# Optimization experiments

Measured on AMD Instinct MI355X. Metric: run time of the kernel, lower is better.

Reference implementation:

```python
import jax, jax.numpy as jnp
import numpy as np

BZ, IN_DIM, STATE_DIM, OUT_DIM, L = 16, 512, 512, 512, 2048
INIT_SCALE = 0.5


def setup_inputs() -> dict:
    key = jax.random.key(0)
    k_u, k_a, k_b, k_c = jax.random.split(key, 4)
    u = jax.random.normal(k_u, (BZ, IN_DIM, L), dtype=jnp.float32)
    A_unconstrained = jax.random.normal(k_a, (STATE_DIM,), dtype=jnp.float32) * 0.1
    B = jax.random.normal(k_b, (STATE_DIM, IN_DIM), dtype=jnp.float32) * INIT_SCALE / np.sqrt(IN_DIM)
    C = jax.random.normal(k_c, (OUT_DIM, STATE_DIM), dtype=jnp.float32) * INIT_SCALE / np.sqrt(STATE_DIM)
    D = jnp.zeros((OUT_DIM, IN_DIM), dtype=jnp.float32)
    h0 = jnp.zeros((STATE_DIM,), dtype=jnp.float32)
    return {"u": u, "A_unconstrained": A_unconstrained, "B": B, "C": C, "D": D, "h0": h0}


def reference(u, A_unconstrained, B, C, D, h0):
    # u: (Bz, input_dim, L)
    Bz = u.shape[0]
    A_diag = -jax.nn.softplus(A_unconstrained)  # (S,)
    # Time-invariant input projection, batched over all timesteps: (L, Bz, S)
    Bu = jnp.einsum('bil,si->lbs', u, B)

    state0 = jnp.broadcast_to(h0[None, :], (Bz, h0.shape[0]))

    def step(state, bu_t):
        x_t = state * A_diag[None, :] + bu_t  # (Bz, S)
        return x_t, x_t

    _, xs = jax.lax.scan(step, state0, Bu)  # xs: (L, Bz, S)

    # Output projection: y_t = C x_t + D u_t  -> (Bz, out, L)
    Y = jnp.einsum('lbs,os->bol', xs, C) + jnp.einsum('bil,oi->bol', u, D)
    return Y
```

## Files before the change

### kernel.cpp

```cpp
#include <hip/hip_runtime.h>
#include <math.h>

typedef __bf16 bf16;
typedef __bf16 bf16x2 __attribute__((ext_vector_type(2)));
typedef __bf16 bf16x4 __attribute__((ext_vector_type(4)));
typedef __bf16 bf16x8 __attribute__((ext_vector_type(8)));
typedef float  f32x4  __attribute__((ext_vector_type(4)));

#define BZd 16
#define INd 512
#define Sd  512
#define Od  512
#define Ld  2048
#define CLd 128
#define NCd (Ld / CLd)

__device__ __forceinline__ int keyf(int r) { return (r & 3) ^ ((r >> 2) & 3); }

__global__ __launch_bounds__(256) void prep_all(const float* __restrict__ B,
                                                const float* __restrict__ C,
                                                const float* __restrict__ D,
                                                const float* __restrict__ Au,
                                                bf16* __restrict__ Bb, bf16* __restrict__ Cb,
                                                bf16* __restrict__ Db, float* __restrict__ A_diag,
                                                int* __restrict__ dfa) {
    __shared__ int sred[4];
    int bid = blockIdx.x;
    if (bid == 768) {
        #pragma unroll
        for (int r = 0; r < 2; ++r) {
            int ss = threadIdx.x + r * 256;
            float x = Au[ss];
            float sp = fmaxf(x, 0.0f) + log1pf(expf(-fabsf(x)));
            A_diag[ss] = -sp;
        }
        return;
    }
    int which = bid >> 8, lb = bid & 255;
    const float* src = which == 0 ? B : (which == 1 ? C : D);
    bf16* dst = which == 0 ? Bb : (which == 1 ? Cb : Db);
    int i = lb * 256 + threadIdx.x;
    f32x4 v = *(const f32x4*)&src[(size_t)i * 4];
    bf16x4 o = { (bf16)v[0], (bf16)v[1], (bf16)v[2], (bf16)v[3] };
    *(bf16x4*)&dst[(size_t)i * 4] = o;
    if (which == 2) {
        int nz = (v[0] != 0.f) | (v[1] != 0.f) | (v[2] != 0.f) | (v[3] != 0.f);
        unsigned long long bl = __ballot(nz);
        int wv = threadIdx.x >> 6;
        if ((threadIdx.x & 63) == 0) sred[wv] = (bl != 0ull);
        __syncthreads();
        if (threadIdx.x == 0) dfa[lb] = sred[0] | sred[1] | sred[2] | sred[3];
    }
}

__global__ __launch_bounds__(256, 2) void gemm_bu128(
    const float* __restrict__ Uf,
    const bf16* __restrict__ Bbf,
    const float* __restrict__ A_diag,
    float* __restrict__ ce,
    bf16* __restrict__ xs)
{
    constexpr int ASLOT = 128 * 32;
    constexpr int BSLOT = 128 * 32;
    __shared__ bf16 lds[2 * ASLOT + 3 * BSLOT];

    const int tid = threadIdx.x, lane = tid & 63, w = tid >> 6;

    int nwg = gridDim.x, bid = blockIdx.x;
    int cpx = nwg >> 3;
    int swz = (bid & 7) * cpx + (bid >> 3);
    int b  = swz >> 6;
    int r0 = swz & 63;
    int by = r0 >> 2;
    int bx = r0 & 3;

    const int wm = w >> 1, wn = w & 1;
    const int fr = lane & 15, g = lane >> 4;
    const int iq = tid & 7, lq = tid >> 3;

    const float* Ub = Uf + (size_t)b * INd * Ld;
    const bf16*  Bp = Bbf + (size_t)(bx * 128) * 512;

    f32x4 acc[4][4];
    #pragma unroll
    for (int i = 0; i < 4; ++i)
        #pragma unroll
        for (int j = 0; j < 4; ++j)
            acc[i][j] = (f32x4){0.f, 0.f, 0.f, 0.f};

    f32x4 areg[4];

    #define GLD16B(srcP, dstElem) __builtin_amdgcn_global_load_lds( \
        (const __attribute__((address_space(1))) void*)(srcP), \
        (__attribute__((address_space(3))) void*)&lds[dstElem], 16, 0, 0)

    auto issueA = [&](int U) {
        #pragma unroll
        for (int d = 0; d < 4; ++d)
            areg[d] = *(const f32x4*)&Ub[(size_t)(U * 32 + iq * 4 + d) * Ld + by * 128 + lq * 4];
    };
    auto writeA = [&](int U) {
        bf16* As = &lds[(U & 1) * ASLOT];
        #pragma unroll
        for (int dl = 0; dl < 4; ++dl) {
            int r = lq * 4 + dl;
            bf16x4 wv = { (bf16)areg[0][dl], (bf16)areg[1][dl], (bf16)areg[2][dl], (bf16)areg[3][dl] };
            *(bf16x4*)&As[r * 32 + (((iq >> 1) ^ keyf(r)) * 8) + (iq & 1) * 4] = wv;
        }
    };
    auto gldB = [&](int U) {
        #pragma unroll
        for (int rb = 0; rb < 2; ++rb) {
            int row = rb * 64 + (tid >> 2);
            int cs = (tid & 3) ^ keyf(row);
            GLD16B(Bp + (size_t)row * 512 + U * 32 + cs * 8,
                   2 * ASLOT + (U % 3) * BSLOT + (rb * 64 + w * 16) * 32);
        }
    };

    issueA(0);
    __builtin_amdgcn_sched_barrier(0);
    gldB(0); gldB(1);
    __builtin_amdgcn_sched_barrier(0);

    for (int U = 0; U < 16; ++U) {
        if (U < 15) { asm volatile("s_waitcnt vmcnt(2)" ::: "memory"); }
        else        { asm volatile("s_waitcnt vmcnt(0)" ::: "memory"); }
        __builtin_amdgcn_sched_barrier(0);
        writeA(U);
        asm volatile("s_waitcnt lgkmcnt(0)" ::: "memory");
        __builtin_amdgcn_sched_barrier(0);
        __builtin_amdgcn_s_barrier();
        __builtin_amdgcn_sched_barrier(0);
        if (U + 1 < 16) {
            issueA(U + 1);
            __builtin_amdgcn_sched_barrier(0);
        }
        bf16x8 av[4], bv[4];
        {
            const bf16* As = &lds[(U & 1) * ASLOT];
            const bf16* Bs = &lds[2 * ASLOT + (U % 3) * BSLOT];
            #pragma unroll
            for (int i = 0; i < 4; ++i) {
                int R = wm * 64 + i * 16 + fr;
                av[i] = *(const bf16x8*)&As[R * 32 + (g ^ keyf(R)) * 8];
            }
            #pragma unroll
            for (int j = 0; j < 4; ++j) {
                int R = wn * 64 + j * 16 + fr;
                bv[j] = *(const bf16x8*)&Bs[R * 32 + (g ^ keyf(R)) * 8];
            }
        }
        if (U + 2 < 16) {
            gldB(U + 2);
            __builtin_amdgcn_sched_barrier(0);
        }
        __builtin_amdgcn_s_setprio(1);
        #pragma unroll
        for (int i = 0; i < 4; ++i)
            #pragma unroll
            for (int j = 0; j < 4; ++j)
                acc[i][j] = __builtin_amdgcn_mfma_f32_16x16x32_bf16(av[i], bv[j], acc[i][j], 0, 0, 0);
        __builtin_amdgcn_s_setprio(0);
    }

    int n0 = bx * 128 + wn * 64 + fr;
    int m0 = by * 128 + wm * 64 + g * 4;

    __syncthreads();
    float* scf = (float*)lds;
    float Sv[4], a64j[4];
    #pragma unroll
    for (int j = 0; j < 4; ++j) {
        float a = A_diag[n0 + j * 16];
        float a2 = a * a, a4 = a2 * a2, a8 = a4 * a4, a16 = a8 * a8;
        float a32 = a16 * a16;
        a64j[j] = a32 * a32;
        float S = 0.f;
        #pragma unroll
        for (int i = 0; i < 4; ++i) {
            f32x4 v = acc[i][j];
            float e = fmaf(fmaf(fmaf(v[0], a, v[1]), a, v[2]), a, v[3]);
            float e0 = __shfl(e, fr), e1 = __shfl(e, fr + 16);
            float e2 = __shfl(e, fr + 32), e3 = __shfl(e, fr + 48);
            float E = fmaf(fmaf(fmaf(e0, a4, e1), a4, e2), a4, e3);
            S = fmaf(S, a16, E);
        }
        Sv[j] = S;
    }
    if (wm == 0 && g == 0) {
        #pragma unroll
        for (int j = 0; j < 4; ++j) scf[wn * 64 + j * 16 + fr] = Sv[j];
    }
    __syncthreads();
    if (wm == 1 && g == 0) {
        #pragma unroll
        for (int j = 0; j < 4; ++j) {
            float S0 = scf[wn * 64 + j * 16 + fr];
            ce[((size_t)b * NCd + by) * Sd + n0 + j * 16] = fmaf(S0, a64j[j], Sv[j]);
        }
    }

    bf16* out = xs + (size_t)b * Ld * Sd;
    #pragma unroll
    for (int i = 0; i < 4; ++i)
        #pragma unroll
        for (int j = 0; j < 4; ++j)
            #pragma unroll
            for (int q = 0; q < 4; ++q)
                out[(size_t)(m0 + i * 16 + q) * Sd + n0 + j * 16] = (bf16)acc[i][j][q];
    #undef GLD16B
}

template<int AREG, int SCAN>
__global__ __launch_bounds__(512, 2) void gemm8p(
    const bf16* __restrict__ Abf, size_t aBS,
    const float* __restrict__ Uf, size_t uBS,
    const bf16* __restrict__ Bbf, size_t bBS,
    const bf16* __restrict__ Dbf,
    const int* __restrict__ dfa,
    const float* __restrict__ A_diag, float* __restrict__ cePtr,
    void* __restrict__ OutV, size_t oBS, int ldOut,
    int NX, int NY)
{
    constexpr int RS   = 32;
    constexpr int ASZ  = 256 * RS;
    constexpr int SLOT = ASZ + 256 * 32;
    __shared__ bf16 lds[4 * SLOT];

    const int tid = threadIdx.x;
    const int lane = tid & 63, w = tid >> 6;

    int nwg = gridDim.x, bid = blockIdx.x;
    int cpx = nwg >> 3;
    int swz = (bid & 7) * cpx + (bid >> 3);
    int pb = NX * NY;
    int b  = swz / pb;
    int r0 = swz - b * pb;
    int by = r0 / NX;
    int bx = r0 - by * NX;

    const int wm = w >> 2, wn = w & 3;
    const int fr = lane & 15, g = lane >> 4;
    const int iq = tid & 7, lq = tid >> 3;

    const bf16*  Ab = Abf + (size_t)b * aBS + (size_t)(by * 256) * 512;
    const float* Ub = Uf ? (Uf + (size_t)b * uBS) : nullptr;
    const bf16*  Bp = Bbf + (size_t)b * bBS + (size_t)(bx * 256) * 512;

    int extra = 0;
    if (dfa) {
        int4 f = ((const int4*)dfa)[lane];
        extra = __any((f.x | f.y | f.z | f.w) != 0) ? 1 : 0;
    }

    f32x4 acc[8][4];
    #pragma unroll
    for (int i = 0; i < 8; ++i)
        #pragma unroll
        for (int j = 0; j < 4; ++j)
            acc[i][j] = (f32x4){0.f, 0.f, 0.f, 0.f};

    #define GLD16(srcP, dstElem) __builtin_amdgcn_global_load_lds( \
        (const __attribute__((address_space(1))) void*)(srcP), \
        (__attribute__((address_space(3))) void*)&lds[dstElem], 16, 0, 0)

    auto gldA = [&](int U) {
        #pragma unroll
        for (int rb = 0; rb < 2; ++rb) {
            int row = rb * 128 + (tid >> 2);
            int cs = (tid & 3) ^ keyf(row);
            GLD16(Ab + (size_t)row * 512 + U * 32 + cs * 8,
                  (U & 3) * SLOT + (rb * 128 + w * 16) * 32);
        }
    };
    auto gldB = [&](int U) {
        #pragma unroll
        for (int rb = 0; rb < 2; ++rb) {
            int row = rb * 128 + (tid >> 2);
            int cs = (tid & 3) ^ keyf(row);
            GLD16(Bp + (size_t)row * 512 + U * 32 + cs * 8,
                  (U & 3) * SLOT + ASZ + (rb * 128 + w * 16) * 32);
        }
    };
    auto readFrags = [&](int slot, bf16x8* avf, bf16x8* bvf) {
        const bf16* As = &lds[slot * SLOT];
        const bf16* Bs = &lds[slot * SLOT + ASZ];
        #pragma unroll
        for (int i = 0; i < 8; ++i) {
            int R = wm * 128 + i * 16 + fr;
            avf[i] = *(const bf16x8*)&As[R * RS + (g ^ keyf(R)) * 8];
        }
        #pragma unroll
        for (int j = 0; j < 4; ++j) {
            int R = wn * 64 + j * 16 + fr;
            bvf[j] = *(const bf16x8*)&Bs[R * 32 + (g ^ keyf(R)) * 8];
        }
    };

    gldA(0); gldB(0); gldA(1); gldB(1);

    for (int U = 0; U < 16; ++U) {
        if (U < 15) { asm volatile("s_waitcnt vmcnt(4)" ::: "memory"); }
        else        { asm volatile("s_waitcnt vmcnt(0)" ::: "memory"); }
        __builtin_amdgcn_sched_barrier(0);
        __builtin_amdgcn_s_barrier();
        __builtin_amdgcn_sched_barrier(0);
        bf16x8 av[8], bv[4];
        readFrags(U & 3, av, bv);
        if (U + 2 < 16) gldA(U + 2);
        if (U + 2 < 16) gldB(U + 2);
        __builtin_amdgcn_s_setprio(1);
        #pragma unroll
        for (int i = 0; i < 8; ++i)
            #pragma unroll
            for (int j = 0; j < 4; ++j)
                acc[i][j] = __builtin_amdgcn_mfma_f32_16x16x32_bf16(av[i], bv[j], acc[i][j], 0, 0, 0);
        __builtin_amdgcn_s_setprio(0);
    }

    if (extra) {
        #pragma unroll 1
        for (int T = 0; T < 16; ++T) {
            int k0 = T * 32;
            __builtin_amdgcn_s_barrier();
            f32x4 r4[4];
            #pragma unroll
            for (int d = 0; d < 4; ++d)
                r4[d] = *(const f32x4*)&Ub[(size_t)(k0 + iq * 4 + d) * Ld + bx * 256 + lq * 4];
            #pragma unroll
            for (int rb = 0; rb < 2; ++rb) {
                int row = rb * 128 + (tid >> 2);
                int cs = (tid & 3) ^ keyf(row);
                GLD16(Dbf + (size_t)(by * 256 + row) * 512 + k0 + cs * 8,
                      (rb * 128 + w * 16) * 32);
            }
            asm volatile("s_waitcnt vmcnt(0)" ::: "memory");
            #pragma unroll
            for (int dl = 0; dl < 4; ++dl) {
                int r = lq * 4 + dl;
                bf16x4 wv = { (bf16)r4[0][dl], (bf16)r4[1][dl], (bf16)r4[2][dl], (bf16)r4[3][dl] };
                int e = ((iq >> 1) ^ keyf(r)) * 8 + (iq & 1) * 4;
                *(bf16x4*)&lds[ASZ + r * 32 + e] = wv;
            }
            asm volatile("s_waitcnt lgkmcnt(0)" ::: "memory");
            __builtin_amdgcn_s_barrier();
            bf16x8 av[8], bv[4];
            readFrags(0, av, bv);
            #pragma unroll
            for (int i = 0; i < 8; ++i)
                #pragma unroll
                for (int j = 0; j < 4; ++j)
                    acc[i][j] = __builtin_amdgcn_mfma_f32_16x16x32_bf16(av[i], bv[j], acc[i][j], 0, 0, 0);
        }
    }

    int n0 = bx * 256 + wn * 64 + fr;
    int m0 = by * 256 + wm * 128 + g * 4;
    float* out = (float*)OutV + (size_t)b * oBS;
    #pragma unroll
    for (int i = 0; i < 8; ++i)
        #pragma unroll
        for (int j = 0; j < 4; ++j)
            #pragma unroll
            for (int q = 0; q < 4; ++q)
                out[(size_t)(m0 + i * 16 + q) * ldOut + n0 + j * 16] = acc[i][j][q];
    #undef GLD16
}

__global__ __launch_bounds__(256) void pass_scan2(bf16* __restrict__ xbuf,
                                                  const float* __restrict__ A_diag,
                                                  const float* __restrict__ ce,
                                                  const float* __restrict__ h0) {
    int gI = blockIdx.x * 256 + threadIdx.x;
    int sp = gI & 255;
    int c = (gI >> 8) & (NCd - 1);
    int b = gI >> 12;
    int s = sp * 2;
    float a0 = A_diag[s], a1 = A_diag[s + 1];
    float acl0 = a0, acl1 = a1;
    #pragma unroll
    for (int i = 0; i < 7; ++i) { acl0 *= acl0; acl1 *= acl1; }
    float x0 = h0[s], x1 = h0[s + 1];
    for (int cp = 0; cp < NCd; ++cp) {
        if (cp >= c) break;
        float2 e = *(const float2*)&ce[((size_t)b * NCd + cp) * Sd + s];
        x0 = fmaf(acl0, x0, e.x);
        x1 = fmaf(acl1, x1, e.y);
    }
    bf16* p = xbuf + ((size_t)b * Ld + (size_t)c * CLd) * Sd + s;
    #pragma unroll 4
    for (int j = 0; j < CLd; ++j) {
        bf16x2 v = *(const bf16x2*)&p[(size_t)j * Sd];
        x0 = fmaf(a0, x0, (float)v[0]);
        x1 = fmaf(a1, x1, (float)v[1]);
        bf16x2 o = { (bf16)x0, (bf16)x1 };
        *(bf16x2*)&p[(size_t)j * Sd] = o;
    }
}

extern "C" void kernel_launch(void* const* d_in, const int* in_sizes, int n_in,
                              void* d_out, int out_size, void* d_ws, size_t ws_size,
                              hipStream_t stream) {
    const float* u  = (const float*)d_in[0];
    const float* Au = (const float*)d_in[1];
    const float* Bm = (const float*)d_in[2];
    const float* Cm = (const float*)d_in[3];
    const float* Dm = (const float*)d_in[4];
    const float* h0 = (const float*)d_in[5];
    float* Y = (float*)d_out;

    char* ws = (char*)d_ws;
    bf16* xs = (bf16*)ws;
    bf16* Bb = (bf16*)(ws + (32ull << 20));
    bf16* Cb = Bb + 262144;
    bf16* Db = Cb + 262144;
    float* A_diag = (float*)(ws + (32ull << 20) + 3ull * 524288);
    float* ce     = A_diag + 512;
    int*   dfa    = (int*)(ce + (size_t)BZd * NCd * Sd);

    prep_all<<<769, 256, 0, stream>>>(Bm, Cm, Dm, Au, Bb, Cb, Db, A_diag, dfa);

    gemm_bu128<<<1024, 256, 0, stream>>>(u, Bb, A_diag, ce, xs);

    pass_scan2<<<(BZd * NCd * (Sd / 2)) / 256, 256, 0, stream>>>(xs, A_diag, ce, h0);

    gemm8p<0, 0><<<(Ld / 256) * (Od / 256) * BZd, 512, 0, stream>>>(
        Cb, 0, u, (size_t)INd * Ld, xs, (size_t)Ld * Sd, Db,
        dfa, A_diag, nullptr,
        (void*)Y, (size_t)Od * Ld, Ld,
        Ld / 256, Od / 256);
}
```

Measured before the change: 100.3 us.

## Deepen GEMM prefetch pipeline with double-buffered A registers and 4-slot B ring

The Bu GEMM now prefetches the fp32 u tile two K-steps ahead using two alternating register sets, and the B ring buffer in LDS grows from 3 to 4 slots. Waits are relaxed from vmcnt(2) to vmcnt(6) so more global loads stay in flight, and launch bounds request 3 workgroups per CU. The aim is to hide global-load latency in the K loop. The extra register set and larger LDS footprint add register and LDS pressure, which may undercut the higher occupancy target. The B ring index change also has to stay correct with the new wait counts.

```diff
diff --git a/kernel.cpp b/kernel.cpp
--- a/kernel.cpp
+++ b/kernel.cpp
@@ -53,7 +53,7 @@
     }
 }
 
-__global__ __launch_bounds__(256, 2) void gemm_bu128(
+__global__ __launch_bounds__(256, 3) void gemm_bu128(
     const float* __restrict__ Uf,
     const bf16* __restrict__ Bbf,
     const float* __restrict__ A_diag,
@@ -62,7 +62,7 @@
 {
     constexpr int ASLOT = 128 * 32;
     constexpr int BSLOT = 128 * 32;
-    __shared__ bf16 lds[2 * ASLOT + 3 * BSLOT];
+    __shared__ bf16 lds[2 * ASLOT + 4 * BSLOT];
 
     const int tid = threadIdx.x, lane = tid & 63, w = tid >> 6;
 
@@ -88,23 +88,23 @@
         for (int j = 0; j < 4; ++j)
             acc[i][j] = (f32x4){0.f, 0.f, 0.f, 0.f};
 
-    f32x4 areg[4];
+    f32x4 pA[4], pB[4];
 
     #define GLD16B(srcP, dstElem) __builtin_amdgcn_global_load_lds( \
         (const __attribute__((address_space(1))) void*)(srcP), \
         (__attribute__((address_space(3))) void*)&lds[dstElem], 16, 0, 0)
 
-    auto issueA = [&](int U) {
+    auto issueA = [&](int U, f32x4 (&dst)[4]) {
         #pragma unroll
         for (int d = 0; d < 4; ++d)
-            areg[d] = *(const f32x4*)&Ub[(size_t)(U * 32 + iq * 4 + d) * Ld + by * 128 + lq * 4];
-    };
-    auto writeA = [&](int U) {
+            dst[d] = *(const f32x4*)&Ub[(size_t)(U * 32 + iq * 4 + d) * Ld + by * 128 + lq * 4];
+    };
+    auto writeA = [&](int U, f32x4 (&src)[4]) {
         bf16* As = &lds[(U & 1) * ASLOT];
         #pragma unroll
         for (int dl = 0; dl < 4; ++dl) {
             int r = lq * 4 + dl;
-            bf16x4 wv = { (bf16)areg[0][dl], (bf16)areg[1][dl], (bf16)areg[2][dl], (bf16)areg[3][dl] };
+            bf16x4 wv = { (bf16)src[0][dl], (bf16)src[1][dl], (bf16)src[2][dl], (bf16)src[3][dl] };
             *(bf16x4*)&As[r * 32 + (((iq >> 1) ^ keyf(r)) * 8) + (iq & 1) * 4] = wv;
         }
     };
@@ -114,32 +114,26 @@
             int row = rb * 64 + (tid >> 2);
             int cs = (tid & 3) ^ keyf(row);
             GLD16B(Bp + (size_t)row * 512 + U * 32 + cs * 8,
-                   2 * ASLOT + (U % 3) * BSLOT + (rb * 64 + w * 16) * 32);
-        }
-    };
-
-    issueA(0);
-    __builtin_amdgcn_sched_barrier(0);
-    gldB(0); gldB(1);
-    __builtin_amdgcn_sched_barrier(0);
-
-    for (int U = 0; U < 16; ++U) {
-        if (U < 15) { asm volatile("s_waitcnt vmcnt(2)" ::: "memory"); }
+                   2 * ASLOT + (U & 3) * BSLOT + (rb * 64 + w * 16) * 32);
+        }
+    };
+    auto step = [&](int U, f32x4 (&cur)[4]) {
+        if (U < 15) { asm volatile("s_waitcnt vmcnt(6)" ::: "memory"); }
         else        { asm volatile("s_waitcnt vmcnt(0)" ::: "memory"); }
         __builtin_amdgcn_sched_barrier(0);
-        writeA(U);
+        writeA(U, cur);
         asm volatile("s_waitcnt lgkmcnt(0)" ::: "memory");
         __builtin_amdgcn_sched_barrier(0);
         __builtin_amdgcn_s_barrier();
         __builtin_amdgcn_sched_barrier(0);
-        if (U + 1 < 16) {
-            issueA(U + 1);
+        if (U + 2 < 16) {
+            issueA(U + 2, cur);
             __builtin_amdgcn_sched_barrier(0);
         }
         bf16x8 av[4], bv[4];
         {
             const bf16* As = &lds[(U & 1) * ASLOT];
-            const bf16* Bs = &lds[2 * ASLOT + (U % 3) * BSLOT];
+            const bf16* Bs = &lds[2 * ASLOT + (U & 3) * BSLOT];
             #pragma unroll
             for (int i = 0; i < 4; ++i) {
                 int R = wm * 64 + i * 16 + fr;
@@ -162,6 +156,22 @@
             for (int j = 0; j < 4; ++j)
                 acc[i][j] = __builtin_amdgcn_mfma_f32_16x16x32_bf16(av[i], bv[j], acc[i][j], 0, 0, 0);
         __builtin_amdgcn_s_setprio(0);
+    };
+
+    issueA(0, pA);
+    __builtin_amdgcn_sched_barrier(0);
+    gldB(0);
+    __builtin_amdgcn_sched_barrier(0);
+    issueA(1, pB);
+    __builtin_amdgcn_sched_barrier(0);
+    gldB(1);
+    __builtin_amdgcn_sched_barrier(0);
+
+    for (int t = 0; t < 4; ++t) {
+        step(4 * t + 0, pA);
+        step(4 * t + 1, pB);
+        step(4 * t + 2, pA);
+        step(4 * t + 3, pB);
     }
 
     int n0 = bx * 128 + wn * 64 + fr;
```

Result: faster. 94.85 us (-5.4%).
